# Optimization experiments

Hardware: AMD Instinct MI355X
Metric: run time of the kernel (lower is better)

The kernel has to match this reference:

```python
import jax, jax.numpy as jnp
import numpy as np

BATCH = 4096
DIM = 512
TEMP = 0.1

def setup_inputs() -> dict:
    key = jax.random.key(0)
    k1, k2 = jax.random.split(key)
    emb_i = jax.random.normal(k1, (BATCH, DIM), dtype=jnp.float32)
    emb_j = jax.random.normal(k2, (BATCH, DIM), dtype=jnp.float32)
    return {"emb_i": emb_i, "emb_j": emb_j}

def _l2_normalize(x, eps=1e-12):
    # matches torch F.normalize(dim=1): x / max(||x||, eps)
    norm = jnp.sqrt(jnp.sum(x * x, axis=1, keepdims=True))
    return x / jnp.maximum(norm, eps)

def reference(emb_i, emb_j):
    n = emb_i.shape[0]
    z_i = _l2_normalize(emb_i)
    z_j = _l2_normalize(emb_j)
    reps = jnp.concatenate([z_i, z_j], axis=0)  # [2N, D], rows unit-norm
    # cosine similarity of unit vectors == dot product -> GEMM instead of O(N^2 D) broadcast
    sim = reps @ reps.T  # [2N, 2N]
    # positives: diag offsets +N and -N
    pos_ij = jnp.sum(z_i * z_j, axis=1)  # diag(sim, +N)
    pos_ji = pos_ij                      # diag(sim, -N) is identical by symmetry
    positives = jnp.concatenate([pos_ij, pos_ji], axis=0)  # [2N]
    nominator = jnp.exp(positives / TEMP)
    neg_mask = 1.0 - jnp.eye(2 * n, dtype=sim.dtype)
    denominator = jnp.sum(neg_mask * jnp.exp(sim / TEMP), axis=1)  # [2N]
    loss_partial = -jnp.log(nominator / denominator)
    return jnp.sum(loss_partial) / (2 * n)
```

## Files before the change

kernel.cpp:

```cpp
#include <hip/hip_runtime.h>
#include <hip/hip_bf16.h>

#define N_ROWS 4096
#define DIM    512
#define M_ROWS 8192
#define BK     32
#define NITER  (DIM / BK)
#define TILE_E (128 * BK)
#define EXP_SCALE 14.4269504088896340736f

typedef unsigned short ushort_t;
typedef __attribute__((ext_vector_type(8))) short short8;
typedef __attribute__((ext_vector_type(4))) float f32x4;

__device__ __forceinline__ ushort_t f2bf(float x) {
  unsigned int bits = __float_as_uint(x);
  unsigned int lsb = (bits >> 16) & 1u;
  bits += 0x7fffu + lsb;
  return (ushort_t)(bits >> 16);
}

__device__ __forceinline__ void store4bf(ushort_t* p, float4 v, float s) {
  union { ushort_t u[4]; uint2 d; } pk;
  pk.u[0] = f2bf(v.x * s);
  pk.u[1] = f2bf(v.y * s);
  pk.u[2] = f2bf(v.z * s);
  pk.u[3] = f2bf(v.w * s);
  *(uint2*)p = pk.d;
}

__device__ __forceinline__ void async16(const ushort_t* g, ushort_t* l) {
  __builtin_amdgcn_global_load_lds(
      (const __attribute__((address_space(1))) void*)g,
      (__attribute__((address_space(3))) void*)l,
      16, 0, 0);
}

__global__ __launch_bounds__(256) void norm_kernel(
    const float* __restrict__ ei, const float* __restrict__ ej,
    ushort_t* __restrict__ reps, float* __restrict__ pos) {
  int b = blockIdx.x * 4 + (threadIdx.x >> 6);
  int lane = threadIdx.x & 63;
  const float4* pi = (const float4*)(ei + (size_t)b * DIM);
  const float4* pj = (const float4*)(ej + (size_t)b * DIM);
  float4 a0 = pi[lane];
  float4 a1 = pi[lane + 64];
  float4 b0 = pj[lane];
  float4 b1 = pj[lane + 64];

  float si = a0.x*a0.x + a0.y*a0.y + a0.z*a0.z + a0.w*a0.w
           + a1.x*a1.x + a1.y*a1.y + a1.z*a1.z + a1.w*a1.w;
  float sj = b0.x*b0.x + b0.y*b0.y + b0.z*b0.z + b0.w*b0.w
           + b1.x*b1.x + b1.y*b1.y + b1.z*b1.z + b1.w*b1.w;
  float dp = a0.x*b0.x + a0.y*b0.y + a0.z*b0.z + a0.w*b0.w
           + a1.x*b1.x + a1.y*b1.y + a1.z*b1.z + a1.w*b1.w;

#pragma unroll
  for (int m = 32; m >= 1; m >>= 1) {
    si += __shfl_xor(si, m, 64);
    sj += __shfl_xor(sj, m, 64);
    dp += __shfl_xor(dp, m, 64);
  }
  float ii = 1.0f / fmaxf(sqrtf(si), 1e-12f);
  float ij = 1.0f / fmaxf(sqrtf(sj), 1e-12f);
  if (lane == 0) pos[b] = dp * ii * ij;

  ushort_t* ri = reps + (size_t)b * DIM;
  ushort_t* rj = reps + (size_t)(b + N_ROWS) * DIM;
  store4bf(ri + lane * 4,       a0, ii);
  store4bf(ri + 256 + lane * 4, a1, ii);
  store4bf(rj + lane * 4,       b0, ij);
  store4bf(rj + 256 + lane * 4, b1, ij);
}

__global__ __launch_bounds__(256) void sim_kernel(
    const ushort_t* __restrict__ reps, float* __restrict__ denom) {
  int t = blockIdx.x;
  int bi = (int)((129.0f - sqrtf((float)(16641 - 8 * t))) * 0.5f);
  while (bi * (129 - bi) / 2 > t) --bi;
  while ((bi + 1) * (128 - bi) / 2 <= t) ++bi;
  int bj = bi + (t - bi * (129 - bi) / 2);

  __shared__ ushort_t As[2][TILE_E];
  __shared__ ushort_t Bs[2][TILE_E];

  int tid  = threadIdx.x;
  int wave = tid >> 6, lane = tid & 63;
  int wr = wave >> 1, wc = wave & 1;
  int quad = lane >> 4, l15 = lane & 15;

  int c0 = wave * 2, c1 = c0 + 1;
  int srow  = lane >> 2;
  int selem = (((lane & 3) ^ (srow & 3)) * 8);
  const ushort_t* gA0 = reps + (size_t)(bi * 128 + c0 * 16 + srow) * DIM + selem;
  const ushort_t* gA1 = reps + (size_t)(bi * 128 + c1 * 16 + srow) * DIM + selem;
  const ushort_t* gB0 = reps + (size_t)(bj * 128 + c0 * 16 + srow) * DIM + selem;
  const ushort_t* gB1 = reps + (size_t)(bj * 128 + c1 * 16 + srow) * DIM + selem;
  int c0o = c0 * 512, c1o = c1 * 512;

  f32x4 zero4 = {0.0f, 0.0f, 0.0f, 0.0f};
  f32x4 acc[4][4];
#pragma unroll
  for (int tr = 0; tr < 4; ++tr)
#pragma unroll
    for (int tc = 0; tc < 4; ++tc) acc[tr][tc] = zero4;

  int sw = (quad ^ (l15 & 3)) * 8;

  async16(gA0, &As[0][c0o]);
  async16(gA1, &As[0][c1o]);
  async16(gB0, &Bs[0][c0o]);
  async16(gB1, &Bs[0][c1o]);

  for (int k = 0; k < NITER; ++k) {
    __syncthreads();
    if (k + 1 < NITER) {
      int off = (k + 1) * BK;
      int nb = (k + 1) & 1;
      async16(gA0 + off, &As[nb][c0o]);
      async16(gA1 + off, &As[nb][c1o]);
      async16(gB0 + off, &Bs[nb][c0o]);
      async16(gB1 + off, &Bs[nb][c1o]);
    }
    int cb = k & 1;
    short8 aF[4], bF[4];
#pragma unroll
    for (int tt = 0; tt < 4; ++tt) {
      aF[tt] = *(const short8*)(&As[cb][(wr * 64 + tt * 16 + l15) * BK + sw]);
      bF[tt] = *(const short8*)(&Bs[cb][(wc * 64 + tt * 16 + l15) * BK + sw]);
    }
#pragma unroll
    for (int tr = 0; tr < 4; ++tr)
#pragma unroll
      for (int tc = 0; tc < 4; ++tc)
        acc[tr][tc] = __builtin_amdgcn_mfma_f32_16x16x32_bf16(
            aF[tr], bF[tc], acc[tr][tc], 0, 0, 0);
  }

  int rowg_base = bi * 128 + wr * 64;
  int colg_base = bj * 128 + wc * 64;

  f32x4 rsum[4];
  float csum[4] = {0.0f, 0.0f, 0.0f, 0.0f};
#pragma unroll
  for (int tr = 0; tr < 4; ++tr) rsum[tr] = zero4;

#pragma unroll
  for (int tr = 0; tr < 4; ++tr) {
    int rowg0 = rowg_base + tr * 16 + quad * 4;
#pragma unroll
    for (int tc = 0; tc < 4; ++tc) {
      int colg = colg_base + tc * 16 + l15;
      f32x4 a = acc[tr][tc];
      f32x4 e;
#pragma unroll
      for (int r = 0; r < 4; ++r) {
        float v = exp2f(a[r] * EXP_SCALE);
        e[r] = ((rowg0 + r) == colg) ? 0.0f : v;
      }
      rsum[tr] += e;
      csum[tc] += e[0] + e[1] + e[2] + e[3];
    }
  }

#pragma unroll
  for (int m = 1; m <= 8; m <<= 1)
#pragma unroll
    for (int tr = 0; tr < 4; ++tr)
#pragma unroll
      for (int r = 0; r < 4; ++r)
        rsum[tr][r] += __shfl_xor(rsum[tr][r], m, 64);

  if (l15 == 0) {
#pragma unroll
    for (int tr = 0; tr < 4; ++tr)
#pragma unroll
      for (int r = 0; r < 4; ++r)
        atomicAdd(&denom[rowg_base + tr * 16 + quad * 4 + r], rsum[tr][r]);
  }

  if (bi != bj) {
#pragma unroll
    for (int m = 16; m <= 32; m <<= 1)
#pragma unroll
      for (int tc = 0; tc < 4; ++tc)
        csum[tc] += __shfl_xor(csum[tc], m, 64);
    if (quad == 0) {
#pragma unroll
      for (int tc = 0; tc < 4; ++tc)
        atomicAdd(&denom[colg_base + tc * 16 + l15], csum[tc]);
    }
  }
}

__global__ __launch_bounds__(1024) void loss_kernel(
    const float* __restrict__ denom, const float* __restrict__ pos,
    float* __restrict__ out) {
  __shared__ float red[16];
  int tid = threadIdx.x;
  float p = 0.0f;
  for (int r = tid; r < M_ROWS; r += 1024)
    p += logf(denom[r]) - pos[r & (N_ROWS - 1)] * 10.0f;
#pragma unroll
  for (int m = 32; m >= 1; m >>= 1) p += __shfl_xor(p, m, 64);
  if ((tid & 63) == 0) red[tid >> 6] = p;
  __syncthreads();
  if (tid == 0) {
    float s = 0.0f;
#pragma unroll
    for (int w = 0; w < 16; ++w) s += red[w];
    out[0] = s * (1.0f / M_ROWS);
  }
}

extern "C" void kernel_launch(void* const* d_in, const int* in_sizes, int n_in,
                              void* d_out, int out_size, void* d_ws, size_t ws_size,
                              hipStream_t stream) {
  const float* ei = (const float*)d_in[0];
  const float* ej = (const float*)d_in[1];
  float* out = (float*)d_out;

  char* ws = (char*)d_ws;
  ushort_t* reps = (ushort_t*)ws;
  float* denom = (float*)(ws + (size_t)M_ROWS * DIM * 2);
  float* pos = (float*)(ws + (size_t)M_ROWS * DIM * 2 + M_ROWS * 4);

  hipMemsetAsync(denom, 0, M_ROWS * sizeof(float), stream);
  norm_kernel<<<N_ROWS / 4, 256, 0, stream>>>(ei, ej, reps, pos);
  sim_kernel<<<2080, 256, 0, stream>>>(reps, denom);
  loss_kernel<<<1, 1024, 0, stream>>>(denom, pos, out);
}
```

Before: 164.1 us.

## Fuse memset and loss reduction into neighbouring kernels, use 2D grid

Zeroing of the denominator buffer and the completion counter moves into the normalisation kernel, replacing the separate memset. The loss reduction moves into the similarity kernel: a global atomic counter picks the last finishing block, which does the final log-sum. The triangular tile index computation becomes a 64x64 grid where lower-triangle blocks exit immediately. The LDS XOR swizzle is also removed, which may add shared-memory bank conflicts on fragment reads in exchange for simpler addressing.

```diff
diff --git a/kernel.cpp b/kernel.cpp
--- a/kernel.cpp
+++ b/kernel.cpp
@@ -7,6 +7,7 @@
 #define BK     32
 #define NITER  (DIM / BK)
 #define TILE_E (128 * BK)
+#define NLIVE  2080
 #define EXP_SCALE 14.4269504088896340736f
 
 typedef unsigned short ushort_t;
@@ -38,9 +39,14 @@
 
 __global__ __launch_bounds__(256) void norm_kernel(
     const float* __restrict__ ei, const float* __restrict__ ej,
-    ushort_t* __restrict__ reps, float* __restrict__ pos) {
-  int b = blockIdx.x * 4 + (threadIdx.x >> 6);
-  int lane = threadIdx.x & 63;
+    ushort_t* __restrict__ reps, float* __restrict__ pos,
+    float* __restrict__ denom, int* __restrict__ counter) {
+  int tid = threadIdx.x;
+  if (blockIdx.x < 32) denom[blockIdx.x * 256 + tid] = 0.0f;
+  if (blockIdx.x == 32 && tid == 0) *counter = 0;
+
+  int b = blockIdx.x * 4 + (tid >> 6);
+  int lane = tid & 63;
   const float4* pi = (const float4*)(ei + (size_t)b * DIM);
   const float4* pj = (const float4*)(ej + (size_t)b * DIM);
   float4 a0 = pi[lane];
@@ -74,12 +80,11 @@
 }
 
 __global__ __launch_bounds__(256) void sim_kernel(
-    const ushort_t* __restrict__ reps, float* __restrict__ denom) {
-  int t = blockIdx.x;
-  int bi = (int)((129.0f - sqrtf((float)(16641 - 8 * t))) * 0.5f);
-  while (bi * (129 - bi) / 2 > t) --bi;
-  while ((bi + 1) * (128 - bi) / 2 <= t) ++bi;
-  int bj = bi + (t - bi * (129 - bi) / 2);
+    const ushort_t* __restrict__ reps, float* __restrict__ denom,
+    const float* __restrict__ pos, float* __restrict__ out,
+    int* __restrict__ counter) {
+  int bj = blockIdx.x, bi = blockIdx.y;
+  if (bi > bj) return;
 
   __shared__ ushort_t As[2][TILE_E];
   __shared__ ushort_t Bs[2][TILE_E];
@@ -91,7 +96,7 @@
 
   int c0 = wave * 2, c1 = c0 + 1;
   int srow  = lane >> 2;
-  int selem = (((lane & 3) ^ (srow & 3)) * 8);
+  int selem = (lane & 3) * 8;
   const ushort_t* gA0 = reps + (size_t)(bi * 128 + c0 * 16 + srow) * DIM + selem;
   const ushort_t* gA1 = reps + (size_t)(bi * 128 + c1 * 16 + srow) * DIM + selem;
   const ushort_t* gB0 = reps + (size_t)(bj * 128 + c0 * 16 + srow) * DIM + selem;
@@ -104,8 +109,6 @@
   for (int tr = 0; tr < 4; ++tr)
 #pragma unroll
     for (int tc = 0; tc < 4; ++tc) acc[tr][tc] = zero4;
-
-  int sw = (quad ^ (l15 & 3)) * 8;
 
   async16(gA0, &As[0][c0o]);
   async16(gA1, &As[0][c1o]);
@@ -126,8 +129,8 @@
     short8 aF[4], bF[4];
 #pragma unroll
     for (int tt = 0; tt < 4; ++tt) {
-      aF[tt] = *(const short8*)(&As[cb][(wr * 64 + tt * 16 + l15) * BK + sw]);
-      bF[tt] = *(const short8*)(&Bs[cb][(wc * 64 + tt * 16 + l15) * BK + sw]);
+      aF[tt] = *(const short8*)(&As[cb][(wr * 64 + tt * 16 + l15) * BK + quad * 8]);
+      bF[tt] = *(const short8*)(&Bs[cb][(wc * 64 + tt * 16 + l15) * BK + quad * 8]);
     }
 #pragma unroll
     for (int tr = 0; tr < 4; ++tr)
@@ -191,25 +194,25 @@
         atomicAdd(&denom[colg_base + tc * 16 + l15], csum[tc]);
     }
   }
-}
-
-__global__ __launch_bounds__(1024) void loss_kernel(
-    const float* __restrict__ denom, const float* __restrict__ pos,
-    float* __restrict__ out) {
-  __shared__ float red[16];
-  int tid = threadIdx.x;
-  float p = 0.0f;
-  for (int r = tid; r < M_ROWS; r += 1024)
-    p += logf(denom[r]) - pos[r & (N_ROWS - 1)] * 10.0f;
-#pragma unroll
-  for (int m = 32; m >= 1; m >>= 1) p += __shfl_xor(p, m, 64);
-  if ((tid & 63) == 0) red[tid >> 6] = p;
+
+  __shared__ int islast;
+  __shared__ float red[4];
+  __threadfence();
   __syncthreads();
-  if (tid == 0) {
-    float s = 0.0f;
-#pragma unroll
-    for (int w = 0; w < 16; ++w) s += red[w];
-    out[0] = s * (1.0f / M_ROWS);
+  if (tid == 0) islast = (atomicAdd(counter, 1) == NLIVE - 1);
+  __syncthreads();
+  if (islast) {
+    float p = 0.0f;
+    for (int r = tid; r < M_ROWS; r += 256) {
+      float v = atomicAdd(&denom[r], 0.0f);
+      p += logf(v) - pos[r & (N_ROWS - 1)] * 10.0f;
+    }
+#pragma unroll
+    for (int m = 32; m >= 1; m >>= 1) p += __shfl_xor(p, m, 64);
+    if ((tid & 63) == 0) red[tid >> 6] = p;
+    __syncthreads();
+    if (tid == 0)
+      out[0] = (red[0] + red[1] + red[2] + red[3]) * (1.0f / M_ROWS);
   }
 }
 
@@ -224,9 +227,8 @@
   ushort_t* reps = (ushort_t*)ws;
   float* denom = (float*)(ws + (size_t)M_ROWS * DIM * 2);
   float* pos = (float*)(ws + (size_t)M_ROWS * DIM * 2 + M_ROWS * 4);
-
-  hipMemsetAsync(denom, 0, M_ROWS * sizeof(float), stream);
-  norm_kernel<<<N_ROWS / 4, 256, 0, stream>>>(ei, ej, reps, pos);
-  sim_kernel<<<2080, 256, 0, stream>>>(reps, denom);
-  loss_kernel<<<1, 1024, 0, stream>>>(denom, pos, out);
-}
+  int* counter = (int*)(ws + (size_t)M_ROWS * DIM * 2 + M_ROWS * 4 + N_ROWS * 4);
+
+  norm_kernel<<<N_ROWS / 4, 256, 0, stream>>>(ei, ej, reps, pos, denom, counter);
+  sim_kernel<<<dim3(64, 64), 256, 0, stream>>>(reps, denom, pos, out, counter);
+}
```

New measurement: 321.8 us. +96.1%, slower.

## Use single-buffered BK=64 GEMM tiles, 2D grid, and fold denom zeroing into norm

Applied to the files above, without the earlier changes.

The similarity kernel's K-step doubles from 32 to 64, and the double-buffered async LDS pipeline becomes a single buffer with a load/sync/compute loop. The aim is fewer barriers and iterations. The LDS XOR swizzle is dropped, the triangular block index decode is replaced by a 64x64 grid whose lower-triangle blocks exit immediately, and the hipMemsetAsync is folded into the normalization kernel. In exchange, global loads no longer overlap MFMA work, unswizzled LDS reads with a 128-byte row stride may cause bank conflicts, and about half the launched blocks do nothing.

```diff
diff --git a/kernel.cpp b/kernel.cpp
--- a/kernel.cpp
+++ b/kernel.cpp
@@ -4,7 +4,7 @@
 #define N_ROWS 4096
 #define DIM    512
 #define M_ROWS 8192
-#define BK     32
+#define BK     64
 #define NITER  (DIM / BK)
 #define TILE_E (128 * BK)
 #define EXP_SCALE 14.4269504088896340736f
@@ -38,9 +38,13 @@
 
 __global__ __launch_bounds__(256) void norm_kernel(
     const float* __restrict__ ei, const float* __restrict__ ej,
-    ushort_t* __restrict__ reps, float* __restrict__ pos) {
-  int b = blockIdx.x * 4 + (threadIdx.x >> 6);
-  int lane = threadIdx.x & 63;
+    ushort_t* __restrict__ reps, float* __restrict__ pos,
+    float* __restrict__ denom) {
+  int tid = threadIdx.x;
+  if (blockIdx.x < 32) denom[blockIdx.x * 256 + tid] = 0.0f;
+
+  int b = blockIdx.x * 4 + (tid >> 6);
+  int lane = tid & 63;
   const float4* pi = (const float4*)(ei + (size_t)b * DIM);
   const float4* pj = (const float4*)(ej + (size_t)b * DIM);
   float4 a0 = pi[lane];
@@ -75,28 +79,31 @@
 
 __global__ __launch_bounds__(256) void sim_kernel(
     const ushort_t* __restrict__ reps, float* __restrict__ denom) {
-  int t = blockIdx.x;
-  int bi = (int)((129.0f - sqrtf((float)(16641 - 8 * t))) * 0.5f);
-  while (bi * (129 - bi) / 2 > t) --bi;
-  while ((bi + 1) * (128 - bi) / 2 <= t) ++bi;
-  int bj = bi + (t - bi * (129 - bi) / 2);
-
-  __shared__ ushort_t As[2][TILE_E];
-  __shared__ ushort_t Bs[2][TILE_E];
+  int bj = blockIdx.x, bi = blockIdx.y;
+  if (bi > bj) return;
+
+  __shared__ ushort_t As[TILE_E];
+  __shared__ ushort_t Bs[TILE_E];
 
   int tid  = threadIdx.x;
   int wave = tid >> 6, lane = tid & 63;
   int wr = wave >> 1, wc = wave & 1;
   int quad = lane >> 4, l15 = lane & 15;
 
-  int c0 = wave * 2, c1 = c0 + 1;
-  int srow  = lane >> 2;
-  int selem = (((lane & 3) ^ (srow & 3)) * 8);
-  const ushort_t* gA0 = reps + (size_t)(bi * 128 + c0 * 16 + srow) * DIM + selem;
-  const ushort_t* gA1 = reps + (size_t)(bi * 128 + c1 * 16 + srow) * DIM + selem;
-  const ushort_t* gB0 = reps + (size_t)(bj * 128 + c0 * 16 + srow) * DIM + selem;
-  const ushort_t* gB1 = reps + (size_t)(bj * 128 + c1 * 16 + srow) * DIM + selem;
-  int c0o = c0 * 512, c1o = c1 * 512;
+  int srow  = lane >> 3;
+  int selem = (lane & 7) * 8;
+  const ushort_t* gA[4];
+  const ushort_t* gB[4];
+  ushort_t* lA[4];
+  ushort_t* lB[4];
+#pragma unroll
+  for (int i = 0; i < 4; ++i) {
+    int c = wave * 4 + i;
+    gA[i] = reps + (size_t)(bi * 128 + c * 8 + srow) * DIM + selem;
+    gB[i] = reps + (size_t)(bj * 128 + c * 8 + srow) * DIM + selem;
+    lA[i] = As + c * 512;
+    lB[i] = Bs + c * 512;
+  }
 
   f32x4 zero4 = {0.0f, 0.0f, 0.0f, 0.0f};
   f32x4 acc[4][4];
@@ -105,36 +112,30 @@
 #pragma unroll
     for (int tc = 0; tc < 4; ++tc) acc[tr][tc] = zero4;
 
-  int sw = (quad ^ (l15 & 3)) * 8;
-
-  async16(gA0, &As[0][c0o]);
-  async16(gA1, &As[0][c1o]);
-  async16(gB0, &Bs[0][c0o]);
-  async16(gB1, &Bs[0][c1o]);
-
-  for (int k = 0; k < NITER; ++k) {
+  for (int kk = 0; kk < DIM; kk += BK) {
     __syncthreads();
-    if (k + 1 < NITER) {
-      int off = (k + 1) * BK;
-      int nb = (k + 1) & 1;
-      async16(gA0 + off, &As[nb][c0o]);
-      async16(gA1 + off, &As[nb][c1o]);
-      async16(gB0 + off, &Bs[nb][c0o]);
-      async16(gB1 + off, &Bs[nb][c1o]);
-    }
-    int cb = k & 1;
-    short8 aF[4], bF[4];
-#pragma unroll
-    for (int tt = 0; tt < 4; ++tt) {
-      aF[tt] = *(const short8*)(&As[cb][(wr * 64 + tt * 16 + l15) * BK + sw]);
-      bF[tt] = *(const short8*)(&Bs[cb][(wc * 64 + tt * 16 + l15) * BK + sw]);
-    }
-#pragma unroll
-    for (int tr = 0; tr < 4; ++tr)
-#pragma unroll
-      for (int tc = 0; tc < 4; ++tc)
-        acc[tr][tc] = __builtin_amdgcn_mfma_f32_16x16x32_bf16(
-            aF[tr], bF[tc], acc[tr][tc], 0, 0, 0);
+#pragma unroll
+    for (int i = 0; i < 4; ++i) {
+      async16(gA[i] + kk, lA[i]);
+      async16(gB[i] + kk, lB[i]);
+    }
+    __syncthreads();
+
+#pragma unroll
+    for (int h = 0; h < 2; ++h) {
+      short8 aF[4], bF[4];
+#pragma unroll
+      for (int tt = 0; tt < 4; ++tt) {
+        aF[tt] = *(const short8*)(&As[(wr * 64 + tt * 16 + l15) * BK + h * 32 + quad * 8]);
+        bF[tt] = *(const short8*)(&Bs[(wc * 64 + tt * 16 + l15) * BK + h * 32 + quad * 8]);
+      }
+#pragma unroll
+      for (int tr = 0; tr < 4; ++tr)
+#pragma unroll
+        for (int tc = 0; tc < 4; ++tc)
+          acc[tr][tc] = __builtin_amdgcn_mfma_f32_16x16x32_bf16(
+              aF[tr], bF[tc], acc[tr][tc], 0, 0, 0);
+    }
   }
 
   int rowg_base = bi * 128 + wr * 64;
@@ -225,8 +226,7 @@
   float* denom = (float*)(ws + (size_t)M_ROWS * DIM * 2);
   float* pos = (float*)(ws + (size_t)M_ROWS * DIM * 2 + M_ROWS * 4);
 
-  hipMemsetAsync(denom, 0, M_ROWS * sizeof(float), stream);
-  norm_kernel<<<N_ROWS / 4, 256, 0, stream>>>(ei, ej, reps, pos);
-  sim_kernel<<<2080, 256, 0, stream>>>(reps, denom);
+  norm_kernel<<<N_ROWS / 4, 256, 0, stream>>>(ei, ej, reps, pos, denom);
+  sim_kernel<<<dim3(64, 64), 256, 0, stream>>>(reps, denom);
   loss_kernel<<<1, 1024, 0, stream>>>(denom, pos, out);
 }
```

New measurement: 177.0 us. 1.08x slower.
